# Kernel optimization log

Hardware: AMD Instinct MI355X
Metric: run time of the kernel (lower is better)

## Reference

```python
import jax, jax.numpy as jnp
import numpy as np

IN_DIM = 16
OUT_DIM = 16
BASIS_DIM = 4
N, M = 4, 96


def setup_inputs() -> dict:
    key = jax.random.key(0)
    k1, k2 = jax.random.split(key)
    x = jax.random.normal(k1, (N, IN_DIM, M), dtype=jnp.float32)
    std = np.sqrt(2.0 / (IN_DIM + OUT_DIM + BASIS_DIM)).astype(np.float32)
    coefs = std * jax.random.normal(k2, (IN_DIM, OUT_DIM, BASIS_DIM), dtype=jnp.float32)
    bias = jnp.zeros((1, OUT_DIM, 1, 1, 1), dtype=jnp.float32)
    return {"x": x, "coefs": coefs, "bias": bias}


def reference(x, coefs, bias):
    # Eq1to3: out[n,s,i,j,k] = sum_d c[d,s,0] x[n,d,i] + c[d,s,1] x[n,d,j]
    #                         + c[d,s,2] x[n,d,k] + c[d,s,3] sum_t x[n,d,t]  + bias
    # Equivalent to einsum('dsb,ndbijk->nsijk', coefs, eset_ops_1_to_3(x)) but
    # without materializing the (n,d,4,m,m,m) basis tensor.
    Y = jnp.einsum('ndi,dsb->nsbi', x, coefs[:, :, :3])        # (n, out, 3, m)
    S = jnp.einsum('nd,ds->ns', x.sum(axis=-1), coefs[:, :, 3])  # (n, out)
    out = (Y[:, :, 0, :, None, None]   # x_i broadcast over j,k
           + Y[:, :, 1, None, :, None]  # x_j broadcast over i,k
           + Y[:, :, 2, None, None, :]  # x_k broadcast over i,j
           + S[:, :, None, None, None]  # set-sum broadcast
           + bias)
    return out  # (n, out_dim, m, m, m)
```

## Files before the change

### kernel.cpp

```cpp
#include <hip/hip_runtime.h>

#define M_DIM   96
#define IN_DIM  16
#define OUT_DIM 16
#define N_BATCH 4

__global__ __launch_bounds__(256) void eq13_kernel(
    const float* __restrict__ x,
    const float* __restrict__ coefs,
    const float* __restrict__ bias,
    float4* __restrict__ out4)
{
    __shared__ float s_y0[M_DIM];
    __shared__ float s_y1[M_DIM];
    __shared__ __align__(16) float s_y2[M_DIM];
    __shared__ float s_red[M_DIM];
    __shared__ float s_S;

    const int bid = blockIdx.x;
    const int ns  = bid / M_DIM;
    const int i   = bid - ns * M_DIM;
    const int n   = ns >> 4;
    const int s   = ns & 15;
    const int t   = threadIdx.x;

    if (t < M_DIM) {
        float y0 = 0.f, y1 = 0.f, y2 = 0.f, y3 = 0.f;
        const float* xb = x + (size_t)n * IN_DIM * M_DIM + t;
        const float* cb = coefs + s * 4;
        #pragma unroll
        for (int d = 0; d < IN_DIM; ++d) {
            float  xv = xb[d * M_DIM];
            float4 c4 = *(const float4*)(cb + d * OUT_DIM * 4);
            y0 = fmaf(xv, c4.x, y0);
            y1 = fmaf(xv, c4.y, y1);
            y2 = fmaf(xv, c4.z, y2);
            y3 = fmaf(xv, c4.w, y3);
        }
        s_y0[t]  = y0;
        s_y1[t]  = y1;
        s_y2[t]  = y2;
        s_red[t] = y3;
    }
    __syncthreads();

    if (t == 0) {
        float ss = 0.f;
        for (int q = 0; q < M_DIM; ++q) ss += s_red[q];
        s_S = ss + bias[s];
    }
    __syncthreads();

    const float  base = s_y0[i] + s_S;
    const float4* y2v = (const float4*)s_y2;
    float4* dst = out4 + (size_t)bid * (M_DIM * M_DIM / 4);

    #pragma unroll
    for (int it = 0; it < 9; ++it) {
        int   c  = t + it * 256;
        int   j  = c / 24;
        int   kq = c - j * 24;
        float v  = base + s_y1[j];
        float4 f = y2v[kq];
        f.x += v; f.y += v; f.z += v; f.w += v;
        dst[c] = f;
    }
}

extern "C" void kernel_launch(void* const* d_in, const int* in_sizes, int n_in,
                              void* d_out, int out_size, void* d_ws, size_t ws_size,
                              hipStream_t stream) {
    const float* x     = (const float*)d_in[0];
    const float* coefs = (const float*)d_in[1];
    const float* bias  = (const float*)d_in[2];
    float4* out4 = (float4*)d_out;

    const int grid = N_BATCH * OUT_DIM * M_DIM;
    eq13_kernel<<<grid, 256, 0, stream>>>(x, coefs, bias, out4);
}
```

Before: 219.4 us.

## Process four i-rows per block with shuffle reduction and nontemporal stores

```diff
diff --git a/kernel.cpp b/kernel.cpp
--- a/kernel.cpp
+++ b/kernel.cpp
@@ -4,12 +4,16 @@
 #define IN_DIM  16
 #define OUT_DIM 16
 #define N_BATCH 4
+#define CHUNK   4
+#define PLANE4  (M_DIM * M_DIM / 4)
+
+typedef float f4 __attribute__((ext_vector_type(4)));
 
 __global__ __launch_bounds__(256) void eq13_kernel(
     const float* __restrict__ x,
     const float* __restrict__ coefs,
     const float* __restrict__ bias,
-    float4* __restrict__ out4)
+    f4* __restrict__ out4)
 {
     __shared__ float s_y0[M_DIM];
     __shared__ float s_y1[M_DIM];
@@ -17,12 +21,13 @@
     __shared__ float s_red[M_DIM];
     __shared__ float s_S;
 
-    const int bid = blockIdx.x;
-    const int ns  = bid / M_DIM;
-    const int i   = bid - ns * M_DIM;
-    const int n   = ns >> 4;
-    const int s   = ns & 15;
-    const int t   = threadIdx.x;
+    const int bid     = blockIdx.x;
+    const int nchunks = M_DIM / CHUNK;
+    const int ns      = bid / nchunks;
+    const int i0      = (bid - ns * nchunks) * CHUNK;
+    const int n       = ns >> 4;
+    const int s       = ns & 15;
+    const int t       = threadIdx.x;
 
     if (t < M_DIM) {
         float y0 = 0.f, y1 = 0.f, y2 = 0.f, y3 = 0.f;
@@ -30,8 +35,8 @@
         const float* cb = coefs + s * 4;
         #pragma unroll
         for (int d = 0; d < IN_DIM; ++d) {
-            float  xv = xb[d * M_DIM];
-            float4 c4 = *(const float4*)(cb + d * OUT_DIM * 4);
+            float xv = xb[d * M_DIM];
+            f4 c4 = *(const f4*)(cb + d * OUT_DIM * 4);
             y0 = fmaf(xv, c4.x, y0);
             y1 = fmaf(xv, c4.y, y1);
             y2 = fmaf(xv, c4.z, y2);
@@ -44,26 +49,34 @@
     }
     __syncthreads();
 
-    if (t == 0) {
-        float ss = 0.f;
-        for (int q = 0; q < M_DIM; ++q) ss += s_red[q];
-        s_S = ss + bias[s];
+    if (t < 64) {
+        float v = s_red[t] + ((t < 32) ? s_red[t + 64] : 0.f);
+        #pragma unroll
+        for (int off = 32; off; off >>= 1) v += __shfl_down(v, off);
+        if (t == 0) s_S = v + bias[s];
     }
     __syncthreads();
 
-    const float  base = s_y0[i] + s_S;
-    const float4* y2v = (const float4*)s_y2;
-    float4* dst = out4 + (size_t)bid * (M_DIM * M_DIM / 4);
+    const float S  = s_S;
+    const float b0 = s_y0[i0 + 0] + S;
+    const float b1 = s_y0[i0 + 1] + S;
+    const float b2 = s_y0[i0 + 2] + S;
+    const float b3 = s_y0[i0 + 3] + S;
+
+    const f4* y2v = (const f4*)s_y2;
+    f4* dst = out4 + (size_t)(ns * M_DIM + i0) * PLANE4;
 
     #pragma unroll
     for (int it = 0; it < 9; ++it) {
         int   c  = t + it * 256;
         int   j  = c / 24;
         int   kq = c - j * 24;
-        float v  = base + s_y1[j];
-        float4 f = y2v[kq];
-        f.x += v; f.y += v; f.z += v; f.w += v;
-        dst[c] = f;
+        float w  = s_y1[j];
+        f4    f  = y2v[kq];
+        __builtin_nontemporal_store(f + (w + b0), dst + c);
+        __builtin_nontemporal_store(f + (w + b1), dst + c + PLANE4);
+        __builtin_nontemporal_store(f + (w + b2), dst + c + 2 * PLANE4);
+        __builtin_nontemporal_store(f + (w + b3), dst + c + 3 * PLANE4);
     }
 }
 
@@ -73,8 +86,8 @@
     const float* x     = (const float*)d_in[0];
     const float* coefs = (const float*)d_in[1];
     const float* bias  = (const float*)d_in[2];
-    float4* out4 = (float4*)d_out;
+    f4* out4 = (f4*)d_out;
 
-    const int grid = N_BATCH * OUT_DIM * M_DIM;
+    const int grid = N_BATCH * OUT_DIM * (M_DIM / CHUNK);
     eq13_kernel<<<grid, 256, 0, stream>>>(x, coefs, bias, out4);
 }
```

After: 231.7 us. 5.6% more time.
